# Kernel tuning notes

Measured on AMD Instinct MI355X. Metric: run time of the kernel, lower is better.

Reference implementation:

```python
import jax, jax.numpy as jnp
import numpy as np

K = 12           # boundary_k
TEMP = 0.75      # logit_temperature


def _knn_idx(p):
    # p: [N,3]; brute-force kNN within one batch element (pointops offsets => per-batch)
    sq = jnp.sum(p * p, axis=-1)
    d2 = sq[:, None] + sq[None, :] - 2.0 * (p @ p.T)   # [N,N]
    _, idx = jax.lax.top_k(-d2, K + 1)                  # self is nearest (d=0)
    return idx[:, 1:]                                    # drop self -> [N,K]


def _mlp2(x, W1, b1, W2, b2, relu_out):
    h = jax.nn.relu(x @ W1 + b1) @ W2 + b2
    return jax.nn.relu(h) if relu_out else h


def setup_inputs() -> dict:
    key = jax.random.key(0)
    ks = jax.random.split(key, 32)
    B, N, C = 4, 4096, 17
    dims = [256, 512, 768]
    RD = 320
    s = 0.02
    inp = {
        'feat0': jax.random.normal(ks[0], (B, N, dims[0]), jnp.float32),
        'feat1': jax.random.normal(ks[1], (B, N, dims[1]), jnp.float32),
        'feat2': jax.random.normal(ks[2], (B, N, dims[2]), jnp.float32),
        'logits': jax.random.normal(ks[3], (B, N, C), jnp.float32),
        'labels': jax.random.randint(ks[4], (B, N), 0, C, jnp.int32),
        'pos': jax.random.normal(ks[5], (B, N, 3), jnp.float32),
    }
    # feat projections
    for i, d in enumerate(dims):
        inp[f'Wp{i}'] = jax.random.normal(ks[6 + i], (d, RD), jnp.float32) * s
        inp[f'bp{i}'] = jnp.zeros((RD,), jnp.float32)
    # boundary encoder 6->96->160
    inp['Wbe1'] = jax.random.normal(ks[10], (6, 96), jnp.float32) * s
    inp['bbe1'] = jnp.zeros((96,), jnp.float32)
    inp['Wbe2'] = jax.random.normal(ks[11], (96, 160), jnp.float32) * s
    inp['bbe2'] = jnp.zeros((160,), jnp.float32)
    # attention (RD+160)->320->n_scales
    inp['Wa1'] = jax.random.normal(ks[12], (RD + 160, 320), jnp.float32) * s
    inp['ba1'] = jnp.zeros((320,), jnp.float32)
    inp['Wa2'] = jax.random.normal(ks[13], (320, 3), jnp.float32) * s
    inp['ba2'] = jnp.zeros((3,), jnp.float32)
    # output proj RD->RD->RD
    inp['Wo1'] = jax.random.normal(ks[14], (RD, RD), jnp.float32) * s
    inp['bo1'] = jnp.zeros((RD,), jnp.float32)
    inp['Wo2'] = jax.random.normal(ks[15], (RD, RD), jnp.float32) * s
    inp['bo2'] = jnp.zeros((RD,), jnp.float32)
    return inp


def boundary_info(logits, labels, pos):
    idx = jax.vmap(_knn_idx)(pos)                          # [B,N,K]
    nb_lab = jax.vmap(lambda l, i: l[i])(labels, idx)      # [B,N,K]
    nb_pos = jax.vmap(lambda p, i: p[i])(pos, idx)         # [B,N,K,3]
    diff = nb_lab != labels[..., None]                     # [B,N,K]
    diff_f = diff.astype(jnp.float32)
    dist = jnp.linalg.norm(nb_pos - pos[:, :, None, :], axis=-1)  # [B,N,K]
    boundary_score = diff_f.mean(axis=-1)
    same = 1.0 - diff_f
    same_dist = (dist * same).sum(-1) / (same.sum(-1) + 1e-6)
    bdist = jnp.min(jnp.where(diff, dist, jnp.inf), axis=-1)
    bdist = jnp.where(jnp.isfinite(bdist), bdist, same_dist)
    mean_d = dist.mean(-1)
    density = 1.0 / (mean_d + 1e-6)
    curvature = jnp.std(dist, axis=-1, ddof=1) / (mean_d + 1e-6)  # torch.std unbiased
    probs = jax.nn.softmax(logits / TEMP, axis=-1)
    confidence = probs.max(-1)
    entropy = -(probs * jnp.log(probs + 1e-8)).sum(-1) / jnp.log(jnp.float32(probs.shape[-1]))
    return jnp.stack([boundary_score, confidence, entropy, density, curvature, bdist], axis=-1)


def reference(feat0, feat1, feat2, logits, labels, pos,
              Wp0, bp0, Wp1, bp1, Wp2, bp2,
              Wbe1, bbe1, Wbe2, bbe2,
              Wa1, ba1, Wa2, ba2,
              Wo1, bo1, Wo2, bo2):
    fp = jnp.stack([feat0 @ Wp0 + bp0, feat1 @ Wp1 + bp1, feat2 @ Wp2 + bp2], axis=2)  # [B,N,3,RD]
    info = boundary_info(logits, labels, pos)                       # [B,N,6]
    enc = _mlp2(info, Wbe1, bbe1, Wbe2, bbe2, relu_out=True)        # [B,N,160]
    global_feat = fp.mean(axis=2)                                   # [B,N,RD]
    attn_in = jnp.concatenate([global_feat, enc], axis=-1)
    attn = jax.nn.softmax(_mlp2(attn_in, Wa1, ba1, Wa2, ba2, relu_out=False), axis=-1)  # [B,N,3]
    fused = (fp * attn[..., None]).sum(axis=2)                      # [B,N,RD]
    out = _mlp2(fused, Wo1, bo1, Wo2, bo2, relu_out=False) + global_feat
    return out, attn
```

## Files before the change

kernel.cpp:

```cpp
#include <hip/hip_runtime.h>
#include <stdint.h>

typedef float fx4 __attribute__((ext_vector_type(4)));
typedef short s8 __attribute__((ext_vector_type(8)));
typedef short s4 __attribute__((ext_vector_type(4)));
typedef unsigned int u32;
typedef u32 ux4 __attribute__((ext_vector_type(4)));

#define MTOT 16384
#define NPTS 4096

#define VMCNT7 asm volatile("s_waitcnt vmcnt(7)" ::: "memory")
#define VMCNT5 asm volatile("s_waitcnt vmcnt(5)" ::: "memory")
#define VMCNT0 asm volatile("s_waitcnt vmcnt(0)" ::: "memory")
#define LGKM0  asm volatile("s_waitcnt lgkmcnt(0)" ::: "memory")
#define SBAR   asm volatile("s_barrier" ::: "memory")
#define SCHED0 __builtin_amdgcn_sched_barrier(0)

__device__ __forceinline__ float b2f(short s) {
    return __uint_as_float(((unsigned)(unsigned short)s) << 16);
}
__device__ __forceinline__ short f2b(float f) {
    unsigned u = __float_as_uint(f);
    u += 0x7fffu + ((u >> 16) & 1u);
    return (short)(u >> 16);
}
__device__ __forceinline__ void g2l16(const void* g, void* l) {
    __builtin_amdgcn_global_load_lds(
        (const __attribute__((address_space(1))) unsigned int*)g,
        (__attribute__((address_space(3))) unsigned int*)l, 16, 0, 0);
}
__device__ __forceinline__ void g2l4(const void* g, void* l) {
    __builtin_amdgcn_global_load_lds(
        (const __attribute__((address_space(1))) unsigned int*)g,
        (__attribute__((address_space(3))) unsigned int*)l, 4, 0, 0);
}

struct WTDesc {
    const float* W[8];
    short* Bt[8];
    int K[8];
    int N[8];
    int Kp[8];
    int swz[8];
    int base[9];
};

__global__ __launch_bounds__(256) void wtrans8_kernel(WTDesc d)
{
    int idx = blockIdx.x * 256 + threadIdx.x;
    if (idx >= d.base[8]) return;
    int s = 0;
#pragma unroll
    for (int t = 1; t < 8; ++t) if (idx >= d.base[t]) s = t;
    int local = idx - d.base[s];
    int N = d.N[s];
    if (d.swz[s]) {
        int c = local / 10240, r = local - c * 10240;
        int n = r >> 5, q = r & 31, slot = q >> 3, t = q & 7;
        int kl = ((slot ^ ((n >> 1) & 3)) << 3) | t;
        int k = c * 32 + kl;
        d.Bt[s][local] = f2b(d.W[s][(size_t)k * N + n]);
    } else {
        int Kp = d.Kp[s], K = d.K[s];
        int n = local / Kp, k = local - n * Kp;
        d.Bt[s][local] = (k < K) ? f2b(d.W[s][(size_t)k * N + n]) : (short)0;
    }
}

__global__ __launch_bounds__(256) void aprep_kernel(
    const float* __restrict__ f0, const float* __restrict__ f1, const float* __restrict__ f2,
    short* __restrict__ a0, short* __restrict__ a1, short* __restrict__ a2)
{
    int g = blockIdx.x * 256 + threadIdx.x;
    const float* src; short* dst; int K; size_t w;
    if (g < 1572864)      { src = f2; dst = a2; K = 768; w = (size_t)g * 8; }
    else if (g < 2621440) { src = f1; dst = a1; K = 512; w = (size_t)(g - 1572864) * 8; }
    else                  { src = f0; dst = a0; K = 256; w = (size_t)(g - 2621440) * 8; }
    int Kt = K * 32;
    int mtile = (int)(w / (size_t)Kt);
    int r2 = (int)(w - (size_t)mtile * Kt);
    int chunk = r2 >> 10;
    int within = r2 & 1023;
    int r = within >> 5, q = within & 31;
    int slot = q >> 3;
    int k = chunk * 32 + ((slot ^ ((r >> 1) & 3)) << 3);
    int row = mtile * 32 + r;
    const float* sp = src + (size_t)row * K + k;
    fx4 v0 = *(const fx4*)sp, v1 = *(const fx4*)(sp + 4);
    s8 o;
    o[0] = f2b(v0[0]); o[1] = f2b(v0[1]); o[2] = f2b(v0[2]); o[3] = f2b(v0[3]);
    o[4] = f2b(v1[0]); o[5] = f2b(v1[1]); o[6] = f2b(v1[2]); o[7] = f2b(v1[3]);
    *(s8*)(dst + w) = o;
}

#define SEGW 132
#define KCAP 40

__global__ __launch_bounds__(512) void knn_part_kernel(
    const float* __restrict__ pos, u32* __restrict__ keys)
{
    __shared__ float xs[8 * SEGW], ys[8 * SEGW], zs[8 * SEGW];
    __shared__ u32 cand[64 * KCAP];
    __shared__ u32 samp[64 * 16];
    __shared__ u32 tauA[64];
    __shared__ int cnt[64];

    int bid = blockIdx.x;
    int b   = bid >> 8;
    int cc  = (bid >> 6) & 3;
    int pch = bid & 63;
    int tid = threadIdx.x;
    int jb  = cc << 10;

    if (tid < 64) cnt[tid] = 0;
    for (int idx = tid; idx < 1024; idx += 512) {
        int seg = idx >> 7, o = idx & 127;
        const float* pp = pos + (size_t)(b * NPTS + jb + idx) * 3;
        xs[seg * SEGW + o] = pp[0];
        ys[seg * SEGW + o] = pp[1];
        zs[seg * SEGW + o] = pp[2];
    }
    __syncthreads();

    int lp = tid >> 3, q = tid & 7;
    int gi = pch * 64 + lp;
    const float* mp = pos + (size_t)(b * NPTS + gi) * 3;
    float mx = mp[0], my = mp[1], mz = mp[2];

    const float* xsq = xs + q * SEGW;
    const float* ysq = ys + q * SEGW;
    const float* zsq = zs + q * SEGW;
    int jg0 = jb + q * 128;

    u32 h0 = 0xFFFFFFFFu, h1v = 0xFFFFFFFFu;
    for (int jj = 0; jj < 128; jj += 4) {
        fx4 xv = *reinterpret_cast<const fx4*>(xsq + jj);
        fx4 yv = *reinterpret_cast<const fx4*>(ysq + jj);
        fx4 zv = *reinterpret_cast<const fx4*>(zsq + jj);
#pragma unroll
        for (int u = 0; u < 4; ++u) {
            float dx = xv[u] - mx, dy = yv[u] - my, dz = zv[u] - mz;
            float d2 = fmaf(dx, dx, fmaf(dy, dy, dz * dz));
            int jg = jg0 + jj + u;
            u32 key = (__float_as_uint(d2) & 0xFFFFF000u) | (u32)jg;
            if (jg == gi) key = 0xFFFFFFFFu;
            u32 lo = (key < h0) ? key : h0;
            u32 hi = (key < h0) ? h0 : key;
            h0 = lo;
            h1v = (hi < h1v) ? hi : h1v;
        }
    }
    samp[lp * 16 + q * 2]     = h0;
    samp[lp * 16 + q * 2 + 1] = h1v;
    __syncthreads();

    {
        ux4 sv0 = *(ux4*)&samp[lp * 16];
        ux4 sv1 = *(ux4*)&samp[lp * 16 + 4];
        ux4 sv2 = *(ux4*)&samp[lp * 16 + 8];
        ux4 sv3 = *(ux4*)&samp[lp * 16 + 12];
        int r0 = 0, r1 = 0;
#pragma unroll
        for (int i = 0; i < 4; ++i) {
            r0 += (sv0[i] < h0) + (sv1[i] < h0) + (sv2[i] < h0) + (sv3[i] < h0);
            r1 += (sv0[i] < h1v) + (sv1[i] < h1v) + (sv2[i] < h1v) + (sv3[i] < h1v);
        }
        if (r0 == 11) tauA[lp] = h0;
        if (r1 == 11) tauA[lp] = h1v;
    }
    __syncthreads();
    u32 tau = tauA[lp];

    for (int jj = 0; jj < 128; jj += 4) {
        fx4 xv = *reinterpret_cast<const fx4*>(xsq + jj);
        fx4 yv = *reinterpret_cast<const fx4*>(ysq + jj);
        fx4 zv = *reinterpret_cast<const fx4*>(zsq + jj);
#pragma unroll
        for (int u = 0; u < 4; ++u) {
            float dx = xv[u] - mx, dy = yv[u] - my, dz = zv[u] - mz;
            float d2 = fmaf(dx, dx, fmaf(dy, dy, dz * dz));
            int jg = jg0 + jj + u;
            u32 key = (__float_as_uint(d2) & 0xFFFFF000u) | (u32)jg;
            if (jg == gi) key = 0xFFFFFFFFu;
            if (key <= tau) {
                int slot = atomicAdd(&cnt[lp], 1);
                if (slot < KCAP) cand[lp * KCAP + slot] = key;
            }
        }
    }
    __syncthreads();

    int n = cnt[lp];
    u32 out[12];
    if (n <= KCAP) {
        u32 e0, e1, e2, e3, e4;
        e0 = (q      < n) ? cand[lp * KCAP + q]      : 0xFFFFFFFFu;
        e1 = (q + 8  < n) ? cand[lp * KCAP + q + 8]  : 0xFFFFFFFFu;
        e2 = (q + 16 < n) ? cand[lp * KCAP + q + 16] : 0xFFFFFFFFu;
        e3 = (q + 24 < n) ? cand[lp * KCAP + q + 24] : 0xFFFFFFFFu;
        e4 = (q + 32 < n) ? cand[lp * KCAP + q + 32] : 0xFFFFFFFFu;
#define CE(a, b) { u32 t0 = (a < b) ? a : b; u32 t1 = (a < b) ? b : a; a = t0; b = t1; }
        CE(e0, e1) CE(e1, e2) CE(e2, e3) CE(e3, e4)
        CE(e0, e1) CE(e1, e2) CE(e2, e3)
        CE(e0, e1) CE(e1, e2)
        CE(e0, e1)
#undef CE
        cand[lp * KCAP + q]      = e0;
        cand[lp * KCAP + q + 8]  = e1;
        cand[lp * KCAP + q + 16] = e2;
        cand[lp * KCAP + q + 24] = e3;
        cand[lp * KCAP + q + 32] = e4;
        int ptr = 0;
        u32 head = e0;
#pragma unroll
        for (int r = 0; r < 12; ++r) {
            u32 m = head;
            u32 o1 = __shfl_xor(m, 4, 8); m = (o1 < m) ? o1 : m;
            u32 o2 = __shfl_xor(m, 2, 8); m = (o2 < m) ? o2 : m;
            u32 o3 = __shfl_xor(m, 1, 8); m = (o3 < m) ? o3 : m;
            if (m == head) {
                ++ptr;
                head = (ptr < 5) ? cand[lp * KCAP + q + ptr * 8] : 0xFFFFFFFFu;
            }
            out[r] = m;
        }
    } else {
        u32 hk[12];
#pragma unroll
        for (int k = 0; k < 12; ++k) hk[k] = 0xFFFFFFFFu;
        for (int jj = 0; jj < 128; jj += 4) {
            fx4 xv = *reinterpret_cast<const fx4*>(xsq + jj);
            fx4 yv = *reinterpret_cast<const fx4*>(ysq + jj);
            fx4 zv = *reinterpret_cast<const fx4*>(zsq + jj);
#pragma unroll
            for (int u = 0; u < 4; ++u) {
                float dx = xv[u] - mx, dy = yv[u] - my, dz = zv[u] - mz;
                float d2 = fmaf(dx, dx, fmaf(dy, dy, dz * dz));
                int jg = jg0 + jj + u;
                u32 key = (__float_as_uint(d2) & 0xFFFFF000u) | (u32)jg;
                if (jg == gi) key = 0xFFFFFFFFu;
                if (key < hk[11]) {
                    hk[11] = key;
#pragma unroll
                    for (int k = 11; k >= 1; --k) {
                        u32 a = hk[k], bb = hk[k - 1];
                        u32 mn = (a < bb) ? a : bb;
                        u32 mxv = (a < bb) ? bb : a;
                        hk[k - 1] = mn; hk[k] = mxv;
                    }
                }
            }
        }
#pragma unroll
        for (int r = 0; r < 12; ++r) {
            u32 m = hk[0];
            u32 o1 = __shfl_xor(m, 4, 8); m = (o1 < m) ? o1 : m;
            u32 o2 = __shfl_xor(m, 2, 8); m = (o2 < m) ? o2 : m;
            u32 o3 = __shfl_xor(m, 1, 8); m = (o3 < m) ? o3 : m;
            if (m == hk[0]) {
#pragma unroll
                for (int k = 0; k < 11; ++k) hk[k] = hk[k + 1];
                hk[11] = 0xFFFFFFFFu;
            }
            out[r] = m;
        }
    }

    size_t kb = ((size_t)(b * NPTS + gi) * 4 + cc) * 12;
    if (q == 0) *reinterpret_cast<ux4*>(&keys[kb])     = (ux4){out[0], out[1], out[2], out[3]};
    if (q == 1) *reinterpret_cast<ux4*>(&keys[kb + 4]) = (ux4){out[4], out[5], out[6], out[7]};
    if (q == 2) *reinterpret_cast<ux4*>(&keys[kb + 8]) = (ux4){out[8], out[9], out[10], out[11]};
}

__global__ __launch_bounds__(256) void knn_merge_kernel(
    const u32* __restrict__ keys, const int* __restrict__ labels,
    const float* __restrict__ logits, float* __restrict__ info32)
{
    __shared__ unsigned char labs[NPTS];
    int b  = blockIdx.x >> 6;
    int pc = blockIdx.x & 63;
    int tid = threadIdx.x;
    for (int idx = tid; idx < NPTS; idx += 256)
        labs[idx] = (unsigned char)labels[b * NPTS + idx];
    __syncthreads();

    int lp = tid >> 2, q = tid & 3;
    int gi = pc * 64 + lp;
    size_t kb = ((size_t)(b * NPTS + gi) * 4 + q) * 12;
    ux4 k0 = *reinterpret_cast<const ux4*>(&keys[kb]);
    ux4 k1 = *reinterpret_cast<const ux4*>(&keys[kb + 4]);
    ux4 k2 = *reinterpret_cast<const ux4*>(&keys[kb + 8]);
    u32 hk[12];
    hk[0] = k0[0]; hk[1] = k0[1]; hk[2] = k0[2]; hk[3] = k0[3];
    hk[4] = k1[0]; hk[5] = k1[1]; hk[6] = k1[2]; hk[7] = k1[3];
    hk[8] = k2[0]; hk[9] = k2[1]; hk[10] = k2[2]; hk[11] = k2[3];

    int mylab = (int)labs[gi];
    float sum_d = 0.f, sum_d2 = 0.f, sum_diff = 0.f, same_d = 0.f, bmin = 3.0e38f;
#pragma unroll
    for (int r = 0; r < 12; ++r) {
        u32 m = hk[0];
        u32 o1 = __shfl_xor(m, 2, 4); m = (o1 < m) ? o1 : m;
        u32 o2 = __shfl_xor(m, 1, 4); m = (o2 < m) ? o2 : m;
        if (m == hk[0]) {
#pragma unroll
            for (int k = 0; k < 11; ++k) hk[k] = hk[k + 1];
            hk[11] = 0xFFFFFFFFu;
        }
        float d = sqrtf(__uint_as_float(m & 0xFFFFF000u));
        int j = (int)(m & 0xFFFu);
        float isdiff = ((int)labs[j] != mylab) ? 1.0f : 0.0f;
        sum_d += d;
        sum_d2 = fmaf(d, d, sum_d2);
        sum_diff += isdiff;
        same_d = fmaf(d, 1.0f - isdiff, same_d);
        if (isdiff > 0.f) bmin = fminf(bmin, d);
    }

    if (q == 0) {
        float nsame = 12.0f - sum_diff;
        float mean_d = sum_d * (1.0f / 12.0f);
        float var = fmaxf(0.f, (sum_d2 - 12.0f * mean_d * mean_d) * (1.0f / 11.0f));
        float md_eps = mean_d + 1e-6f;
        float curvature = sqrtf(var) / md_eps;
        float density = 1.0f / md_eps;
        float same_dist = same_d / (nsame + 1e-6f);
        float bdist = (bmin < 2.9e38f) ? bmin : same_dist;
        float bscore = sum_diff * (1.0f / 12.0f);

        const float* lg = logits + (size_t)(b * NPTS + gi) * 17;
        float v[17];
        float vmax = -3.0e38f;
#pragma unroll
        for (int c = 0; c < 17; ++c) { v[c] = lg[c] * (1.0f / 0.75f); vmax = fmaxf(vmax, v[c]); }
        float ssum = 0.f;
#pragma unroll
        for (int c = 0; c < 17; ++c) { v[c] = expf(v[c] - vmax); ssum += v[c]; }
        float inv = 1.0f / ssum;
        float conf = 0.f, ent = 0.f;
#pragma unroll
        for (int c = 0; c < 17; ++c) {
            float pprob = v[c] * inv;
            conf = fmaxf(conf, pprob);
            ent += pprob * logf(pprob + 1e-8f);
        }
        ent = -ent * (1.0f / 2.8332133f);

        float* op = info32 + (size_t)(b * NPTS + gi) * 32;
        fx4 o0 = {bscore, conf, ent, density};
        fx4 o1v = {curvature, bdist, 0.f, 0.f};
        fx4 zz = {0.f, 0.f, 0.f, 0.f};
        *reinterpret_cast<fx4*>(op + 0)  = o0;
        *reinterpret_cast<fx4*>(op + 4)  = o1v;
        *reinterpret_cast<fx4*>(op + 8)  = zz;
        *reinterpret_cast<fx4*>(op + 12) = zz;
        *reinterpret_cast<fx4*>(op + 16) = zz;
        *reinterpret_cast<fx4*>(op + 20) = zz;
        *reinterpret_cast<fx4*>(op + 24) = zz;
        *reinterpret_cast<fx4*>(op + 28) = zz;
    }
}

template<bool AF32, bool RELU, bool NMASK, bool ADDF, bool OUTF, bool OUTB>
__global__ __launch_bounds__(256) void gemm_k(
    const void* __restrict__ Ap, int lda,
    const short* __restrict__ Bt,
    const float* __restrict__ bias,
    float* __restrict__ Cf, int ldcf,
    short* __restrict__ Cb, int ldcb, int cboff,
    const float* __restrict__ Af, int ldaf,
    int N, int K, int ntiles)
{
    __shared__ short As[128 * 40];
    __shared__ short Bs[64 * 40];
    int bid = blockIdx.x;
    int mt = bid / ntiles, nt = bid - mt * ntiles;
    int m0 = mt * 128, n0 = nt * 64;
    int tid = threadIdx.x, l = tid & 63, wid = tid >> 6;
    int wm = wid & 1, wn = wid >> 1, lr = l & 15, lh = l >> 4;
    fx4 acc[4][2] = {};

    int nsteps = K >> 5;
    for (int kt = 0; kt < nsteps; ++kt) {
        int k0 = kt << 5;
        if constexpr (AF32) {
            const float* A = (const float*)Ap;
#pragma unroll
            for (int it = 0; it < 4; ++it) {
                int tt = tid + it * 256;
                int row = tt >> 3, seg = tt & 7;
                fx4 vv = *reinterpret_cast<const fx4*>(A + (size_t)(m0 + row) * lda + k0 + seg * 4);
                s4 w; w[0] = f2b(vv[0]); w[1] = f2b(vv[1]); w[2] = f2b(vv[2]); w[3] = f2b(vv[3]);
                *reinterpret_cast<s4*>(&As[row * 40 + seg * 4]) = w;
            }
        } else {
            const short* A = (const short*)Ap;
#pragma unroll
            for (int it = 0; it < 2; ++it) {
                int tt = tid + it * 256;
                int row = tt >> 2, seg = tt & 3;
                s8 vv = *reinterpret_cast<const s8*>(A + (size_t)(m0 + row) * lda + k0 + seg * 8);
                *reinterpret_cast<s8*>(&As[row * 40 + seg * 8]) = vv;
            }
        }
        {
            int row = tid >> 2, seg = tid & 3;
            s8 vb = {0, 0, 0, 0, 0, 0, 0, 0};
            if (!NMASK || (n0 + row) < N)
                vb = *reinterpret_cast<const s8*>(Bt + (size_t)(n0 + row) * K + k0 + seg * 8);
            *reinterpret_cast<s8*>(&Bs[row * 40 + seg * 8]) = vb;
        }
        __syncthreads();
        s8 af[4], bfr[2];
#pragma unroll
        for (int mf = 0; mf < 4; ++mf)
            af[mf] = *reinterpret_cast<s8*>(&As[(wm * 64 + mf * 16 + lr) * 40 + lh * 8]);
#pragma unroll
        for (int nf = 0; nf < 2; ++nf)
            bfr[nf] = *reinterpret_cast<s8*>(&Bs[(wn * 32 + nf * 16 + lr) * 40 + lh * 8]);
#pragma unroll
        for (int mf = 0; mf < 4; ++mf)
#pragma unroll
            for (int nf = 0; nf < 2; ++nf)
                acc[mf][nf] = __builtin_amdgcn_mfma_f32_16x16x32_bf16(af[mf], bfr[nf], acc[mf][nf], 0, 0, 0);
        __syncthreads();
    }

#pragma unroll
    for (int nf = 0; nf < 2; ++nf) {
        int col = n0 + wn * 32 + nf * 16 + lr;
        if (NMASK && col >= N) continue;
        float bv = bias[col];
#pragma unroll
        for (int mf = 0; mf < 4; ++mf) {
            int r0 = m0 + wm * 64 + mf * 16 + lh * 4;
#pragma unroll
            for (int rg = 0; rg < 4; ++rg) {
                float c = acc[mf][nf][rg] + bv;
                if (RELU) c = fmaxf(c, 0.0f);
                int row = r0 + rg;
                if constexpr (ADDF) c += Af[(size_t)row * ldaf + col];
                if constexpr (OUTF) Cf[(size_t)row * ldcf + col] = c;
                if constexpr (OUTB) Cb[(size_t)row * ldcb + cboff + col] = f2b(c);
            }
        }
    }
}

__global__ __launch_bounds__(256, 2) void mega_kernel(
    const short* __restrict__ at0, const short* __restrict__ at1, const short* __restrict__ at2,
    const short* __restrict__ btp0, const short* __restrict__ btp1, const short* __restrict__ btp2,
    const float* __restrict__ bp0, const float* __restrict__ bp1, const float* __restrict__ bp2,
    const short* __restrict__ bta1, const float* __restrict__ ba1,
    const float* __restrict__ Wa2, const float* __restrict__ ba2,
    const short* __restrict__ bto1, const float* __restrict__ bo1,
    const short* __restrict__ bto2, const float* __restrict__ bo2,
    const short* __restrict__ encb,
    float* __restrict__ outf, float* __restrict__ attn_out)
{
    __shared__ alignas(16) short smem[38144];
    char* smb = (char*)smem;
    constexpr int BB0 = 0, BB1 = 20480, AB0 = 40960, AB1 = 43008, R2B = 45056, SWF = 75776;
    float* smf = (float*)(smb + SWF);

    int tid = threadIdx.x, l = tid & 63, wid = tid >> 6;
    int lr = l & 15, lh = l >> 4;
    int m0 = blockIdx.x * 32;

    auto stageB = [&](int bbase, const short* btg, int kt) {
#pragma unroll
        for (int r = 0; r < 5; ++r) {
            int idx = tid + r * 256;
            g2l16(btg + (size_t)kt * 10240 + idx * 8, smb + bbase + idx * 16);
        }
    };
    auto stageA = [&](int abase, const short* atgm, int kt) {
        const short* src = atgm + (size_t)kt * 1024;
        g2l4(src + tid * 2,       smb + abase + tid * 4);
        g2l4(src + 512 + tid * 2, smb + abase + 1024 + tid * 4);
    };
    auto readB = [&](int bbase, s8* bf) {
#pragma unroll
        for (int nf = 0; nf < 5; ++nf) {
            int row = wid * 80 + nf * 16 + lr;
            bf[nf] = *(const s8*)(smb + bbase + row * 64 + ((lh ^ ((row >> 1) & 3)) << 4));
        }
    };
    auto readAp = [&](int abase, s8* af) {
#pragma unroll
        for (int mf = 0; mf < 2; ++mf) {
            int row = mf * 16 + lr;
            af[mf] = *(const s8*)(smb + abase + row * 64 + ((lh ^ ((row >> 1) & 3)) << 4));
        }
    };

    fx4 gacc[2][5] = {};

    auto do_proj = [&](const short* atgm, const short* btg, int ns,
                       const float* bias, s4 (&fpks)[2][5]) {
        fx4 acc[2][5] = {};
        stageB(BB0, btg, 0); stageA(AB0, atgm, 0);
        stageB(BB1, btg, 1); stageA(AB1, atgm, 1);
        LGKM0;
#pragma unroll 1
        for (int kt = 0; kt < ns; ++kt) {
            if (kt < ns - 1) { VMCNT7; } else { VMCNT0; }
            SBAR;
            int cb = (kt & 1) ? BB1 : BB0;
            int ca = (kt & 1) ? AB1 : AB0;
            s8 af[2], bf[5];
            readAp(ca, af);
            readB(cb, bf);
            LGKM0; SCHED0;
            SBAR;
            if (kt + 2 < ns) { stageB(cb, btg, kt + 2); stageA(ca, atgm, kt + 2); }
#pragma unroll
            for (int mf = 0; mf < 2; ++mf)
#pragma unroll
                for (int nf = 0; nf < 5; ++nf)
                    acc[mf][nf] = __builtin_amdgcn_mfma_f32_16x16x32_bf16(af[mf], bf[nf], acc[mf][nf], 0, 0, 0);
        }
#pragma unroll
        for (int nf = 0; nf < 5; ++nf) {
            float bv = bias[wid * 80 + nf * 16 + lr];
#pragma unroll
            for (int mf = 0; mf < 2; ++mf) {
                s4 pk;
#pragma unroll
                for (int rg = 0; rg < 4; ++rg) {
                    float c = acc[mf][nf][rg] + bv;
                    gacc[mf][nf][rg] += c;
                    pk[rg] = f2b(c);
                }
                fpks[mf][nf] = pk;
            }
        }
    };

    s4 fpk0[2][5], fpk1[2][5], fpk2[2][5];
    do_proj(at2 + (size_t)blockIdx.x * 24576, btp2, 24, bp2, fpk2);
    do_proj(at1 + (size_t)blockIdx.x * 16384, btp1, 16, bp1, fpk1);
    do_proj(at0 + (size_t)blockIdx.x * 8192,  btp0, 8,  bp0, fpk0);

#pragma unroll
    for (int nf = 0; nf < 5; ++nf) {
        int col = wid * 80 + nf * 16 + lr;
#pragma unroll
        for (int mf = 0; mf < 2; ++mf)
#pragma unroll
            for (int rg = 0; rg < 4; ++rg) {
                int row = mf * 16 + lh * 4 + rg;
                int bir = (col * 2) ^ (((row >> 1) & 3) << 4);
                *(short*)(smb + R2B + row * 960 + bir) = f2b(gacc[mf][nf][rg] * (1.0f / 3.0f));
            }
    }
#pragma unroll
    for (int r = 0; r < 3; ++r) {
        int idx = tid + r * 256;
        if (idx < 640) {
            int row = idx / 20, sg = idx - row * 20;
            s8 v = *reinterpret_cast<const s8*>(encb + (size_t)(m0 + row) * 160 + sg * 8);
            int bir = (640 + sg * 16) ^ (((row >> 1) & 3) << 4);
            *(s8*)(smb + R2B + row * 960 + bir) = v;
        }
    }

    auto do_gemm2 = [&](const short* btg, int ns, fx4 acc[2][5]) {
        stageB(BB0, btg, 0);
        stageB(BB1, btg, 1);
        LGKM0;
#pragma unroll 1
        for (int kt = 0; kt < ns; ++kt) {
            if (kt < ns - 1) { VMCNT5; } else { VMCNT0; }
            SBAR;
            int cb = (kt & 1) ? BB1 : BB0;
            s8 af[2], bf[5];
#pragma unroll
            for (int mf = 0; mf < 2; ++mf) {
                int row = mf * 16 + lr;
                int bir = (kt * 64 + (lh << 4)) ^ (((row >> 1) & 3) << 4);
                af[mf] = *(const s8*)(smb + R2B + row * 960 + bir);
            }
            readB(cb, bf);
            LGKM0; SCHED0;
            SBAR;
            if (kt + 2 < ns) stageB(cb, btg, kt + 2);
#pragma unroll
            for (int mf = 0; mf < 2; ++mf)
#pragma unroll
                for (int nf = 0; nf < 5; ++nf)
                    acc[mf][nf] = __builtin_amdgcn_mfma_f32_16x16x32_bf16(af[mf], bf[nf], acc[mf][nf], 0, 0, 0);
        }
    };

    {
        fx4 acc1[2][5] = {};
        do_gemm2(bta1, 15, acc1);
#pragma unroll
        for (int nf = 0; nf < 5; ++nf) {
            int col = wid * 80 + nf * 16 + lr;
            float bv = ba1[col];
#pragma unroll
            for (int mf = 0; mf < 2; ++mf)
#pragma unroll
                for (int rg = 0; rg < 4; ++rg) {
                    int row = mf * 16 + lh * 4 + rg;
                    int bir = (col * 2) ^ (((row >> 1) & 3) << 4);
                    *(short*)(smb + R2B + row * 960 + bir) = f2b(fmaxf(acc1[mf][nf][rg] + bv, 0.0f));
                }
        }
    }

    {
        float* ws2 = (float*)smb;
        if (tid < 240)
            reinterpret_cast<fx4*>(ws2)[tid] = reinterpret_cast<const fx4*>(Wa2)[tid];
        __syncthreads();
        int row = tid >> 3, g = tid & 7;
        float l0 = 0.f, l1 = 0.f, l2 = 0.f;
#pragma unroll
        for (int j = 0; j < 5; ++j) {
            int bir = (g * 80 + j * 16) ^ (((row >> 1) & 3) << 4);
            s8 v = *(const s8*)(smb + R2B + row * 960 + bir);
#pragma unroll
            for (int u = 0; u < 8; ++u) {
                float f = b2f(v[u]);
                const float* wp = ws2 + (g * 40 + j * 8 + u) * 3;
                l0 = fmaf(f, wp[0], l0);
                l1 = fmaf(f, wp[1], l1);
                l2 = fmaf(f, wp[2], l2);
            }
        }
#pragma unroll
        for (int s = 4; s >= 1; s >>= 1) {
            l0 += __shfl_xor(l0, s, 8);
            l1 += __shfl_xor(l1, s, 8);
            l2 += __shfl_xor(l2, s, 8);
        }
        if (g == 0) {
            l0 += ba2[0]; l1 += ba2[1]; l2 += ba2[2];
            float mx = fmaxf(l0, fmaxf(l1, l2));
            float e0 = expf(l0 - mx), e1 = expf(l1 - mx), e2 = expf(l2 - mx);
            float inv = 1.0f / (e0 + e1 + e2);
            float w0 = e0 * inv, w1 = e1 * inv, w2 = e2 * inv;
            attn_out[(size_t)(m0 + row) * 3 + 0] = w0;
            attn_out[(size_t)(m0 + row) * 3 + 1] = w1;
            attn_out[(size_t)(m0 + row) * 3 + 2] = w2;
            smf[row * 4 + 0] = w0; smf[row * 4 + 1] = w1; smf[row * 4 + 2] = w2;
        }
        __syncthreads();
    }

#pragma unroll
    for (int mf = 0; mf < 2; ++mf)
#pragma unroll
        for (int rg = 0; rg < 4; ++rg) {
            int row = mf * 16 + lh * 4 + rg;
            float w0 = smf[row * 4 + 0], w1 = smf[row * 4 + 1], w2 = smf[row * 4 + 2];
#pragma unroll
            for (int nf = 0; nf < 5; ++nf) {
                int col = wid * 80 + nf * 16 + lr;
                float fv = w0 * b2f(fpk0[mf][nf][rg])
                         + w1 * b2f(fpk1[mf][nf][rg])
                         + w2 * b2f(fpk2[mf][nf][rg]);
                int bir = (col * 2) ^ (((row >> 1) & 3) << 4);
                *(short*)(smb + R2B + row * 960 + bir) = f2b(fv);
            }
        }

    {
        fx4 acch[2][5] = {};
        do_gemm2(bto1, 10, acch);
#pragma unroll
        for (int nf = 0; nf < 5; ++nf) {
            int col = wid * 80 + nf * 16 + lr;
            float bv = bo1[col];
#pragma unroll
            for (int mf = 0; mf < 2; ++mf)
#pragma unroll
                for (int rg = 0; rg < 4; ++rg) {
                    int row = mf * 16 + lh * 4 + rg;
                    int bir = (col * 2) ^ (((row >> 1) & 3) << 4);
                    *(short*)(smb + R2B + row * 960 + bir) = f2b(fmaxf(acch[mf][nf][rg] + bv, 0.0f));
                }
        }
    }

    {
        fx4 acco[2][5] = {};
        do_gemm2(bto2, 10, acco);
#pragma unroll
        for (int nf = 0; nf < 5; ++nf) {
            int col = wid * 80 + nf * 16 + lr;
            float bv = bo2[col];
#pragma unroll
            for (int mf = 0; mf < 2; ++mf)
#pragma unroll
                for (int rg = 0; rg < 4; ++rg) {
                    int row = m0 + mf * 16 + lh * 4 + rg;
                    float c = acco[mf][nf][rg] + bv + gacc[mf][nf][rg] * (1.0f / 3.0f);
                    outf[(size_t)row * 320 + col] = c;
                }
        }
    }
}

extern "C" void kernel_launch(void* const* d_in, const int* in_sizes, int n_in,
                              void* d_out, int out_size, void* d_ws, size_t ws_size,
                              hipStream_t stream)
{
    const float* feat0  = (const float*)d_in[0];
    const float* feat1  = (const float*)d_in[1];
    const float* feat2  = (const float*)d_in[2];
    const float* logits = (const float*)d_in[3];
    const int*   labels = (const int*)d_in[4];
    const float* pos    = (const float*)d_in[5];
    const float* Wp0 = (const float*)d_in[6];   const float* bp0 = (const float*)d_in[7];
    const float* Wp1 = (const float*)d_in[8];   const float* bp1 = (const float*)d_in[9];
    const float* Wp2 = (const float*)d_in[10];  const float* bp2 = (const float*)d_in[11];
    const float* Wbe1 = (const float*)d_in[12]; const float* bbe1 = (const float*)d_in[13];
    const float* Wbe2 = (const float*)d_in[14]; const float* bbe2 = (const float*)d_in[15];
    const float* Wa1 = (const float*)d_in[16];  const float* ba1 = (const float*)d_in[17];
    const float* Wa2 = (const float*)d_in[18];  const float* ba2 = (const float*)d_in[19];
    const float* Wo1 = (const float*)d_in[20];  const float* bo1 = (const float*)d_in[21];
    const float* Wo2 = (const float*)d_in[22];  const float* bo2 = (const float*)d_in[23];

    char* p = (char*)d_ws;
    auto alloc = [&](size_t bytes) { char* r = p; p += (bytes + 255) & ~(size_t)255; return r; };
    short* bt_p0  = (short*)alloc((size_t)320 * 256 * 2);
    short* bt_p1  = (short*)alloc((size_t)320 * 512 * 2);
    short* bt_p2  = (short*)alloc((size_t)320 * 768 * 2);
    short* bt_be1 = (short*)alloc((size_t)96 * 32 * 2);
    short* bt_be2 = (short*)alloc((size_t)160 * 96 * 2);
    short* bt_a1  = (short*)alloc((size_t)320 * 480 * 2);
    short* bt_o1  = (short*)alloc((size_t)320 * 320 * 2);
    short* bt_o2  = (short*)alloc((size_t)320 * 320 * 2);
    float* info32 = (float*)alloc((size_t)MTOT * 32 * 4);
    short* h1     = (short*)alloc((size_t)MTOT * 96 * 2);
    short* encb   = (short*)alloc((size_t)MTOT * 160 * 2);
    u32*   knnkeys= (u32*)alloc((size_t)MTOT * 4 * 12 * 4);
    short* abt0   = (short*)alloc((size_t)MTOT * 256 * 2);
    short* abt1   = (short*)alloc((size_t)MTOT * 512 * 2);
    short* abt2   = (short*)alloc((size_t)MTOT * 768 * 2);

    float* outf = (float*)d_out;
    float* attn_out = outf + (size_t)MTOT * 320;

    WTDesc wd;
    const float* Ws[8] = {Wp0, Wp1, Wp2, Wbe1, Wbe2, Wa1, Wo1, Wo2};
    short* Bts[8] = {bt_p0, bt_p1, bt_p2, bt_be1, bt_be2, bt_a1, bt_o1, bt_o2};
    int Ks[8]  = {256, 512, 768, 6, 96, 480, 320, 320};
    int Ns[8]  = {320, 320, 320, 96, 160, 320, 320, 320};
    int Kps[8] = {256, 512, 768, 32, 96, 480, 320, 320};
    int Sz[8]  = {1, 1, 1, 0, 0, 1, 1, 1};
    int acc = 0;
    for (int s = 0; s < 8; ++s) {
        wd.W[s] = Ws[s]; wd.Bt[s] = Bts[s];
        wd.K[s] = Ks[s]; wd.N[s] = Ns[s]; wd.Kp[s] = Kps[s]; wd.swz[s] = Sz[s];
        wd.base[s] = acc;
        acc += Ns[s] * Kps[s];
    }
    wd.base[8] = acc;
    wtrans8_kernel<<<(acc + 255) / 256, 256, 0, stream>>>(wd);

    knn_part_kernel<<<1024, 512, 0, stream>>>(pos, knnkeys);
    knn_merge_kernel<<<256, 256, 0, stream>>>(knnkeys, labels, logits, info32);

    gemm_k<true, true, true, false, false, true><<<256, 256, 0, stream>>>(
        info32, 32, bt_be1, bbe1, nullptr, 0, h1, 96, 0, nullptr, 0, 96, 32, 2);
    gemm_k<false, true, true, false, false, true><<<384, 256, 0, stream>>>(
        h1, 96, bt_be2, bbe2, nullptr, 0, encb, 160, 0, nullptr, 0, 160, 96, 3);

    aprep_kernel<<<12288, 256, 0, stream>>>(feat0, feat1, feat2, abt0, abt1, abt2);

    mega_kernel<<<512, 256, 0, stream>>>(
        abt0, abt1, abt2,
        bt_p0, bt_p1, bt_p2,
        bp0, bp1, bp2,
        bt_a1, ba1, Wa2, ba2,
        bt_o1, bo1, bt_o2, bo2,
        encb, outf, attn_out);
}
```

Measured before the change: 160.0 us.

## Enlarge mega kernel tile to 64 rows, triple-buffer, and fuse aprep into kNN launch

The mega kernel now runs 512 threads on a 64-row tile. Its 8 waves are split 2x4 over M and N, so each B-weight tile staged into LDS is reused across twice as many rows. The K-loop moves from double to triple buffering, which drops the second barrier per iteration and adjusts the vmcnt waits to match. The bf16 A-prep conversion, with its layout re-tiled for 64-row tiles, is merged into the kNN partition kernel as extra blocks to save a launch and overlap with kNN work. The cost is much larger LDS (about 133 KB per block) and fewer resident blocks, only 256 blocks total, which may leave CUs underused.

```diff
diff --git a/kernel.cpp b/kernel.cpp
--- a/kernel.cpp
+++ b/kernel.cpp
@@ -10,8 +10,8 @@
 #define MTOT 16384
 #define NPTS 4096
 
-#define VMCNT7 asm volatile("s_waitcnt vmcnt(7)" ::: "memory")
-#define VMCNT5 asm volatile("s_waitcnt vmcnt(5)" ::: "memory")
+#define VMCNT6 asm volatile("s_waitcnt vmcnt(6)" ::: "memory")
+#define VMCNT4 asm volatile("s_waitcnt vmcnt(4)" ::: "memory")
 #define VMCNT0 asm volatile("s_waitcnt vmcnt(0)" ::: "memory")
 #define LGKM0  asm volatile("s_waitcnt lgkmcnt(0)" ::: "memory")
 #define SBAR   asm volatile("s_barrier" ::: "memory")
@@ -68,43 +68,43 @@
     }
 }
 
-__global__ __launch_bounds__(256) void aprep_kernel(
+#define SEGW 132
+#define KCAP 40
+
+__global__ __launch_bounds__(512) void knap_kernel(
+    const float* __restrict__ pos, u32* __restrict__ keys,
     const float* __restrict__ f0, const float* __restrict__ f1, const float* __restrict__ f2,
     short* __restrict__ a0, short* __restrict__ a1, short* __restrict__ a2)
-{
-    int g = blockIdx.x * 256 + threadIdx.x;
-    const float* src; short* dst; int K; size_t w;
-    if (g < 1572864)      { src = f2; dst = a2; K = 768; w = (size_t)g * 8; }
-    else if (g < 2621440) { src = f1; dst = a1; K = 512; w = (size_t)(g - 1572864) * 8; }
-    else                  { src = f0; dst = a0; K = 256; w = (size_t)(g - 2621440) * 8; }
-    int Kt = K * 32;
-    int mtile = (int)(w / (size_t)Kt);
-    int r2 = (int)(w - (size_t)mtile * Kt);
-    int chunk = r2 >> 10;
-    int within = r2 & 1023;
-    int r = within >> 5, q = within & 31;
-    int slot = q >> 3;
-    int k = chunk * 32 + ((slot ^ ((r >> 1) & 3)) << 3);
-    int row = mtile * 32 + r;
-    const float* sp = src + (size_t)row * K + k;
-    fx4 v0 = *(const fx4*)sp, v1 = *(const fx4*)(sp + 4);
-    s8 o;
-    o[0] = f2b(v0[0]); o[1] = f2b(v0[1]); o[2] = f2b(v0[2]); o[3] = f2b(v0[3]);
-    o[4] = f2b(v1[0]); o[5] = f2b(v1[1]); o[6] = f2b(v1[2]); o[7] = f2b(v1[3]);
-    *(s8*)(dst + w) = o;
-}
-
-#define SEGW 132
-#define KCAP 40
-
-__global__ __launch_bounds__(512) void knn_part_kernel(
-    const float* __restrict__ pos, u32* __restrict__ keys)
 {
     __shared__ float xs[8 * SEGW], ys[8 * SEGW], zs[8 * SEGW];
     __shared__ u32 cand[64 * KCAP];
     __shared__ u32 samp[64 * 16];
     __shared__ u32 tauA[64];
     __shared__ int cnt[64];
+
+    if (blockIdx.x >= 1024) {
+        int g = (blockIdx.x - 1024) * 512 + threadIdx.x;
+        const float* src; short* dst; int K; size_t w;
+        if (g < 1572864)      { src = f2; dst = a2; K = 768; w = (size_t)g * 8; }
+        else if (g < 2621440) { src = f1; dst = a1; K = 512; w = (size_t)(g - 1572864) * 8; }
+        else                  { src = f0; dst = a0; K = 256; w = (size_t)(g - 2621440) * 8; }
+        int Kt = K * 64;
+        int mtile = (int)(w / (size_t)Kt);
+        int r2 = (int)(w - (size_t)mtile * Kt);
+        int chunk = r2 >> 11;
+        int within = r2 & 2047;
+        int r = within >> 5, q = within & 31;
+        int slot = q >> 3;
+        int k = chunk * 32 + ((slot ^ ((r >> 1) & 3)) << 3);
+        int row = mtile * 64 + r;
+        const float* sp = src + (size_t)row * K + k;
+        fx4 v0 = *(const fx4*)sp, v1 = *(const fx4*)(sp + 4);
+        s8 o;
+        o[0] = f2b(v0[0]); o[1] = f2b(v0[1]); o[2] = f2b(v0[2]); o[3] = f2b(v0[3]);
+        o[4] = f2b(v1[0]); o[5] = f2b(v1[1]); o[6] = f2b(v1[2]); o[7] = f2b(v1[3]);
+        *(s8*)(dst + w) = o;
+        return;
+    }
 
     int bid = blockIdx.x;
     int b   = bid >> 8;
@@ -448,7 +448,7 @@
     }
 }
 
-__global__ __launch_bounds__(256, 2) void mega_kernel(
+__global__ __launch_bounds__(512, 2) void mega_kernel(
     const short* __restrict__ at0, const short* __restrict__ at1, const short* __restrict__ at2,
     const short* __restrict__ btp0, const short* __restrict__ btp1, const short* __restrict__ btp2,
     const float* __restrict__ bp0, const float* __restrict__ bp1, const float* __restrict__ bp2,
@@ -459,38 +459,45 @@
     const short* __restrict__ encb,
     float* __restrict__ outf, float* __restrict__ attn_out)
 {
-    __shared__ alignas(16) short smem[38144];
-    char* smb = (char*)smem;
-    constexpr int BB0 = 0, BB1 = 20480, AB0 = 40960, AB1 = 43008, R2B = 45056, SWF = 75776;
+    __shared__ alignas(16) char smb[136192];
+    const int BBo[3] = {0, 20480, 40960};
+    const int ABo[3] = {61440, 65536, 69632};
+    constexpr int R2B = 73728, SWF = 135168;
     float* smf = (float*)(smb + SWF);
 
-    int tid = threadIdx.x, l = tid & 63, wid = tid >> 6;
-    int lr = l & 15, lh = l >> 4;
-    int m0 = blockIdx.x * 32;
+    int tid = threadIdx.x, wid = tid >> 6, l = tid & 63;
+    int wm = wid >> 2, wn = wid & 3, lr = l & 15, lh = l >> 4;
+    int m0 = blockIdx.x * 64;
 
     auto stageB = [&](int bbase, const short* btg, int kt) {
-#pragma unroll
-        for (int r = 0; r < 5; ++r) {
-            int idx = tid + r * 256;
-            g2l16(btg + (size_t)kt * 10240 + idx * 8, smb + bbase + idx * 16);
-        }
+        const char* s = (const char*)(btg + (size_t)kt * 10240);
+        int o1 = wid * 1024 + l * 16;
+        int o2 = 8192 + o1;
+        int o3 = 16384 + wid * 256 + l * 4;
+        int o4 = 2048 + o3;
+        g2l16(s + o1, smb + bbase + o1);
+        g2l16(s + o2, smb + bbase + o2);
+        g2l4(s + o3, smb + bbase + o3);
+        g2l4(s + o4, smb + bbase + o4);
     };
     auto stageA = [&](int abase, const short* atgm, int kt) {
-        const short* src = atgm + (size_t)kt * 1024;
-        g2l4(src + tid * 2,       smb + abase + tid * 4);
-        g2l4(src + 512 + tid * 2, smb + abase + 1024 + tid * 4);
+        const char* s = (const char*)(atgm + (size_t)kt * 2048);
+        int o1 = wid * 256 + l * 4;
+        int o2 = 2048 + o1;
+        g2l4(s + o1, smb + abase + o1);
+        g2l4(s + o2, smb + abase + o2);
     };
     auto readB = [&](int bbase, s8* bf) {
 #pragma unroll
         for (int nf = 0; nf < 5; ++nf) {
-            int row = wid * 80 + nf * 16 + lr;
+            int row = wn * 80 + nf * 16 + lr;
             bf[nf] = *(const s8*)(smb + bbase + row * 64 + ((lh ^ ((row >> 1) & 3)) << 4));
         }
     };
-    auto readAp = [&](int abase, s8* af) {
+    auto readA = [&](int abase, s8* af) {
 #pragma unroll
         for (int mf = 0; mf < 2; ++mf) {
-            int row = mf * 16 + lr;
+            int row = wm * 32 + mf * 16 + lr;
             af[mf] = *(const s8*)(smb + abase + row * 64 + ((lh ^ ((row >> 1) & 3)) << 4));
         }
     };
@@ -500,30 +507,33 @@
     auto do_proj = [&](const short* atgm, const short* btg, int ns,
                        const float* bias, s4 (&fpks)[2][5]) {
         fx4 acc[2][5] = {};
-        stageB(BB0, btg, 0); stageA(AB0, atgm, 0);
-        stageB(BB1, btg, 1); stageA(AB1, atgm, 1);
+        stageB(BBo[0], btg, 0); stageA(ABo[0], atgm, 0);
+        stageB(BBo[1], btg, 1); stageA(ABo[1], atgm, 1);
         LGKM0;
 #pragma unroll 1
         for (int kt = 0; kt < ns; ++kt) {
-            if (kt < ns - 1) { VMCNT7; } else { VMCNT0; }
+            if (kt < ns - 1) { VMCNT6; } else { VMCNT0; }
             SBAR;
-            int cb = (kt & 1) ? BB1 : BB0;
-            int ca = (kt & 1) ? AB1 : AB0;
+            int ph = kt - (kt / 3) * 3;
             s8 af[2], bf[5];
-            readAp(ca, af);
-            readB(cb, bf);
-            LGKM0; SCHED0;
-            SBAR;
-            if (kt + 2 < ns) { stageB(cb, btg, kt + 2); stageA(ca, atgm, kt + 2); }
+            readA(ABo[ph], af);
+            readB(BBo[ph], bf);
+            if (kt + 2 < ns) {
+                int p2 = (kt + 2) - ((kt + 2) / 3) * 3;
+                stageB(BBo[p2], btg, kt + 2);
+                stageA(ABo[p2], atgm, kt + 2);
+            }
 #pragma unroll
             for (int mf = 0; mf < 2; ++mf)
 #pragma unroll
                 for (int nf = 0; nf < 5; ++nf)
                     acc[mf][nf] = __builtin_amdgcn_mfma_f32_16x16x32_bf16(af[mf], bf[nf], acc[mf][nf], 0, 0, 0);
-        }
+            SCHED0; LGKM0;
+        }
+        SBAR;
 #pragma unroll
         for (int nf = 0; nf < 5; ++nf) {
-            float bv = bias[wid * 80 + nf * 16 + lr];
+            float bv = bias[wn * 80 + nf * 16 + lr];
 #pragma unroll
             for (int mf = 0; mf < 2; ++mf) {
                 s4 pk;
@@ -539,26 +549,26 @@
     };
 
     s4 fpk0[2][5], fpk1[2][5], fpk2[2][5];
-    do_proj(at2 + (size_t)blockIdx.x * 24576, btp2, 24, bp2, fpk2);
-    do_proj(at1 + (size_t)blockIdx.x * 16384, btp1, 16, bp1, fpk1);
-    do_proj(at0 + (size_t)blockIdx.x * 8192,  btp0, 8,  bp0, fpk0);
+    do_proj(at2 + (size_t)blockIdx.x * 49152, btp2, 24, bp2, fpk2);
+    do_proj(at1 + (size_t)blockIdx.x * 32768, btp1, 16, bp1, fpk1);
+    do_proj(at0 + (size_t)blockIdx.x * 16384, btp0, 8,  bp0, fpk0);
 
 #pragma unroll
     for (int nf = 0; nf < 5; ++nf) {
-        int col = wid * 80 + nf * 16 + lr;
+        int col = wn * 80 + nf * 16 + lr;
 #pragma unroll
         for (int mf = 0; mf < 2; ++mf)
 #pragma unroll
             for (int rg = 0; rg < 4; ++rg) {
-                int row = mf * 16 + lh * 4 + rg;
+                int row = wm * 32 + mf * 16 + lh * 4 + rg;
                 int bir = (col * 2) ^ (((row >> 1) & 3) << 4);
                 *(short*)(smb + R2B + row * 960 + bir) = f2b(gacc[mf][nf][rg] * (1.0f / 3.0f));
             }
     }
 #pragma unroll
     for (int r = 0; r < 3; ++r) {
-        int idx = tid + r * 256;
-        if (idx < 640) {
+        int idx = tid + r * 512;
+        if (idx < 1280) {
             int row = idx / 20, sg = idx - row * 20;
             s8 v = *reinterpret_cast<const s8*>(encb + (size_t)(m0 + row) * 160 + sg * 8);
             int bir = (640 + sg * 16) ^ (((row >> 1) & 3) << 4);
@@ -566,32 +576,35 @@
         }
     }
 
-    auto do_gemm2 = [&](const short* btg, int ns, fx4 acc[2][5]) {
-        stageB(BB0, btg, 0);
-        stageB(BB1, btg, 1);
+    auto do_gemm2 = [&](const short* btg, int ns, fx4 (&acc)[2][5]) {
+        stageB(BBo[0], btg, 0);
+        stageB(BBo[1], btg, 1);
         LGKM0;
 #pragma unroll 1
         for (int kt = 0; kt < ns; ++kt) {
-            if (kt < ns - 1) { VMCNT5; } else { VMCNT0; }
+            if (kt < ns - 1) { VMCNT4; } else { VMCNT0; }
             SBAR;
-            int cb = (kt & 1) ? BB1 : BB0;
+            int ph = kt - (kt / 3) * 3;
             s8 af[2], bf[5];
 #pragma unroll
             for (int mf = 0; mf < 2; ++mf) {
-                int row = mf * 16 + lr;
+                int row = wm * 32 + mf * 16 + lr;
                 int bir = (kt * 64 + (lh << 4)) ^ (((row >> 1) & 3) << 4);
                 af[mf] = *(const s8*)(smb + R2B + row * 960 + bir);
             }
-            readB(cb, bf);
-            LGKM0; SCHED0;
-            SBAR;
-            if (kt + 2 < ns) stageB(cb, btg, kt + 2);
+            readB(BBo[ph], bf);
+            if (kt + 2 < ns) {
+                int p2 = (kt + 2) - ((kt + 2) / 3) * 3;
+                stageB(BBo[p2], btg, kt + 2);
+            }
 #pragma unroll
             for (int mf = 0; mf < 2; ++mf)
 #pragma unroll
                 for (int nf = 0; nf < 5; ++nf)
                     acc[mf][nf] = __builtin_amdgcn_mfma_f32_16x16x32_bf16(af[mf], bf[nf], acc[mf][nf], 0, 0, 0);
-        }
+            SCHED0; LGKM0;
+        }
+        SBAR;
     };
 
     {
@@ -599,13 +612,13 @@
         do_gemm2(bta1, 15, acc1);
 #pragma unroll
         for (int nf = 0; nf < 5; ++nf) {
-            int col = wid * 80 + nf * 16 + lr;
+            int col = wn * 80 + nf * 16 + lr;
             float bv = ba1[col];
 #pragma unroll
             for (int mf = 0; mf < 2; ++mf)
 #pragma unroll
                 for (int rg = 0; rg < 4; ++rg) {
-                    int row = mf * 16 + lh * 4 + rg;
+                    int row = wm * 32 + mf * 16 + lh * 4 + rg;
                     int bir = (col * 2) ^ (((row >> 1) & 3) << 4);
                     *(short*)(smb + R2B + row * 960 + bir) = f2b(fmaxf(acc1[mf][nf][rg] + bv, 0.0f));
                 }
@@ -656,11 +669,11 @@
     for (int mf = 0; mf < 2; ++mf)
 #pragma unroll
         for (int rg = 0; rg < 4; ++rg) {
-            int row = mf * 16 + lh * 4 + rg;
+            int row = wm * 32 + mf * 16 + lh * 4 + rg;
             float w0 = smf[row * 4 + 0], w1 = smf[row * 4 + 1], w2 = smf[row * 4 + 2];
 #pragma unroll
             for (int nf = 0; nf < 5; ++nf) {
-                int col = wid * 80 + nf * 16 + lr;
+                int col = wn * 80 + nf * 16 + lr;
                 float fv = w0 * b2f(fpk0[mf][nf][rg])
                          + w1 * b2f(fpk1[mf][nf][rg])
                          + w2 * b2f(fpk2[mf][nf][rg]);
@@ -674,13 +687,13 @@
         do_gemm2(bto1, 10, acch);
 #pragma unroll
         for (int nf = 0; nf < 5; ++nf) {
-            int col = wid * 80 + nf * 16 + lr;
+            int col = wn * 80 + nf * 16 + lr;
             float bv = bo1[col];
 #pragma unroll
             for (int mf = 0; mf < 2; ++mf)
 #pragma unroll
                 for (int rg = 0; rg < 4; ++rg) {
-                    int row = mf * 16 + lh * 4 + rg;
+                    int row = wm * 32 + mf * 16 + lh * 4 + rg;
                     int bir = (col * 2) ^ (((row >> 1) & 3) << 4);
                     *(short*)(smb + R2B + row * 960 + bir) = f2b(fmaxf(acch[mf][nf][rg] + bv, 0.0f));
                 }
@@ -692,13 +705,13 @@
         do_gemm2(bto2, 10, acco);
 #pragma unroll
         for (int nf = 0; nf < 5; ++nf) {
-            int col = wid * 80 + nf * 16 + lr;
+            int col = wn * 80 + nf * 16 + lr;
             float bv = bo2[col];
 #pragma unroll
             for (int mf = 0; mf < 2; ++mf)
 #pragma unroll
                 for (int rg = 0; rg < 4; ++rg) {
-                    int row = m0 + mf * 16 + lh * 4 + rg;
+                    int row = m0 + wm * 32 + mf * 16 + lh * 4 + rg;
                     float c = acco[mf][nf][rg] + bv + gacc[mf][nf][rg] * (1.0f / 3.0f);
                     outf[(size_t)row * 320 + col] = c;
                 }
@@ -764,7 +777,9 @@
     wd.base[8] = acc;
     wtrans8_kernel<<<(acc + 255) / 256, 256, 0, stream>>>(wd);
 
-    knn_part_kernel<<<1024, 512, 0, stream>>>(pos, knnkeys);
+    knap_kernel<<<7168, 512, 0, stream>>>(pos, knnkeys,
+                                          feat0, feat1, feat2,
+                                          abt0, abt1, abt2);
     knn_merge_kernel<<<256, 256, 0, stream>>>(knnkeys, labels, logits, info32);
 
     gemm_k<true, true, true, false, false, true><<<256, 256, 0, stream>>>(
@@ -772,9 +787,7 @@
     gemm_k<false, true, true, false, false, true><<<384, 256, 0, stream>>>(
         h1, 96, bt_be2, bbe2, nullptr, 0, encb, 160, 0, nullptr, 0, 160, 96, 3);
 
-    aprep_kernel<<<12288, 256, 0, stream>>>(feat0, feat1, feat2, abt0, abt1, abt2);
-
-    mega_kernel<<<512, 256, 0, stream>>>(
+    mega_kernel<<<256, 512, 0, stream>>>(
         abt0, abt1, abt2,
         bt_p0, bt_p1, bt_p2,
         bp0, bp1, bp2,
```

Measured after the change: 155.0 us. 3.1% less time.

## Merge aprep into kNN partition kernel and spill projection fragments to global

Applied to the files above, without the earlier changes.

The bf16 feature-repack work (aprep) now runs as extra blocks appended to the kNN partition kernel, so both jobs share one launch and the memory-bound conversion can overlap the compute-bound kNN. In the mega kernel, the three per-scale projection fragments are written to a per-thread global scratch buffer instead of being held in registers, and read back later for the attention-weighted fusion. This is meant to cut register pressure and raise occupancy, at the cost of extra global traffic and larger shared-memory footprint for the aprep blocks, which now carry the kNN kernel's static LDS.

```diff
diff --git a/kernel.cpp b/kernel.cpp
--- a/kernel.cpp
+++ b/kernel.cpp
@@ -68,43 +68,43 @@
     }
 }
 
-__global__ __launch_bounds__(256) void aprep_kernel(
+#define SEGW 132
+#define KCAP 40
+
+__global__ __launch_bounds__(512) void knap_kernel(
+    const float* __restrict__ pos, u32* __restrict__ keys,
     const float* __restrict__ f0, const float* __restrict__ f1, const float* __restrict__ f2,
     short* __restrict__ a0, short* __restrict__ a1, short* __restrict__ a2)
-{
-    int g = blockIdx.x * 256 + threadIdx.x;
-    const float* src; short* dst; int K; size_t w;
-    if (g < 1572864)      { src = f2; dst = a2; K = 768; w = (size_t)g * 8; }
-    else if (g < 2621440) { src = f1; dst = a1; K = 512; w = (size_t)(g - 1572864) * 8; }
-    else                  { src = f0; dst = a0; K = 256; w = (size_t)(g - 2621440) * 8; }
-    int Kt = K * 32;
-    int mtile = (int)(w / (size_t)Kt);
-    int r2 = (int)(w - (size_t)mtile * Kt);
-    int chunk = r2 >> 10;
-    int within = r2 & 1023;
-    int r = within >> 5, q = within & 31;
-    int slot = q >> 3;
-    int k = chunk * 32 + ((slot ^ ((r >> 1) & 3)) << 3);
-    int row = mtile * 32 + r;
-    const float* sp = src + (size_t)row * K + k;
-    fx4 v0 = *(const fx4*)sp, v1 = *(const fx4*)(sp + 4);
-    s8 o;
-    o[0] = f2b(v0[0]); o[1] = f2b(v0[1]); o[2] = f2b(v0[2]); o[3] = f2b(v0[3]);
-    o[4] = f2b(v1[0]); o[5] = f2b(v1[1]); o[6] = f2b(v1[2]); o[7] = f2b(v1[3]);
-    *(s8*)(dst + w) = o;
-}
-
-#define SEGW 132
-#define KCAP 40
-
-__global__ __launch_bounds__(512) void knn_part_kernel(
-    const float* __restrict__ pos, u32* __restrict__ keys)
 {
     __shared__ float xs[8 * SEGW], ys[8 * SEGW], zs[8 * SEGW];
     __shared__ u32 cand[64 * KCAP];
     __shared__ u32 samp[64 * 16];
     __shared__ u32 tauA[64];
     __shared__ int cnt[64];
+
+    if (blockIdx.x >= 1024) {
+        int g = (blockIdx.x - 1024) * 512 + threadIdx.x;
+        const float* src; short* dst; int K; size_t w;
+        if (g < 1572864)      { src = f2; dst = a2; K = 768; w = (size_t)g * 8; }
+        else if (g < 2621440) { src = f1; dst = a1; K = 512; w = (size_t)(g - 1572864) * 8; }
+        else                  { src = f0; dst = a0; K = 256; w = (size_t)(g - 2621440) * 8; }
+        int Kt = K * 32;
+        int mtile = (int)(w / (size_t)Kt);
+        int r2 = (int)(w - (size_t)mtile * Kt);
+        int chunk = r2 >> 10;
+        int within = r2 & 1023;
+        int r = within >> 5, q = within & 31;
+        int slot = q >> 3;
+        int k = chunk * 32 + ((slot ^ ((r >> 1) & 3)) << 3);
+        int row = mtile * 32 + r;
+        const float* sp = src + (size_t)row * K + k;
+        fx4 v0 = *(const fx4*)sp, v1 = *(const fx4*)(sp + 4);
+        s8 o;
+        o[0] = f2b(v0[0]); o[1] = f2b(v0[1]); o[2] = f2b(v0[2]); o[3] = f2b(v0[3]);
+        o[4] = f2b(v1[0]); o[5] = f2b(v1[1]); o[6] = f2b(v1[2]); o[7] = f2b(v1[3]);
+        *(s8*)(dst + w) = o;
+        return;
+    }
 
     int bid = blockIdx.x;
     int b   = bid >> 8;
@@ -456,17 +456,19 @@
     const float* __restrict__ Wa2, const float* __restrict__ ba2,
     const short* __restrict__ bto1, const float* __restrict__ bo1,
     const short* __restrict__ bto2, const float* __restrict__ bo2,
-    const short* __restrict__ encb,
+    const short* __restrict__ encb, short* __restrict__ fpb,
     float* __restrict__ outf, float* __restrict__ attn_out)
 {
     __shared__ alignas(16) short smem[38144];
     char* smb = (char*)smem;
     constexpr int BB0 = 0, BB1 = 20480, AB0 = 40960, AB1 = 43008, R2B = 45056, SWF = 75776;
+    constexpr size_t FPS = (size_t)512 * 256 * 40;
     float* smf = (float*)(smb + SWF);
 
     int tid = threadIdx.x, l = tid & 63, wid = tid >> 6;
     int lr = l & 15, lh = l >> 4;
     int m0 = blockIdx.x * 32;
+    short* fpt = fpb + (size_t)(blockIdx.x * 256 + tid) * 40;
 
     auto stageB = [&](int bbase, const short* btg, int kt) {
 #pragma unroll
@@ -498,7 +500,7 @@
     fx4 gacc[2][5] = {};
 
     auto do_proj = [&](const short* atgm, const short* btg, int ns,
-                       const float* bias, s4 (&fpks)[2][5]) {
+                       const float* bias, short* fpo) {
         fx4 acc[2][5] = {};
         stageB(BB0, btg, 0); stageA(AB0, atgm, 0);
         stageB(BB1, btg, 1); stageA(AB1, atgm, 1);
@@ -533,15 +535,14 @@
                     gacc[mf][nf][rg] += c;
                     pk[rg] = f2b(c);
                 }
-                fpks[mf][nf] = pk;
+                *(s4*)(fpo + (mf * 5 + nf) * 4) = pk;
             }
         }
     };
 
-    s4 fpk0[2][5], fpk1[2][5], fpk2[2][5];
-    do_proj(at2 + (size_t)blockIdx.x * 24576, btp2, 24, bp2, fpk2);
-    do_proj(at1 + (size_t)blockIdx.x * 16384, btp1, 16, bp1, fpk1);
-    do_proj(at0 + (size_t)blockIdx.x * 8192,  btp0, 8,  bp0, fpk0);
+    do_proj(at2 + (size_t)blockIdx.x * 24576, btp2, 24, bp2, fpt + 2 * FPS);
+    do_proj(at1 + (size_t)blockIdx.x * 16384, btp1, 16, bp1, fpt + 1 * FPS);
+    do_proj(at0 + (size_t)blockIdx.x * 8192,  btp0, 8,  bp0, fpt);
 
 #pragma unroll
     for (int nf = 0; nf < 5; ++nf) {
@@ -566,7 +567,7 @@
         }
     }
 
-    auto do_gemm2 = [&](const short* btg, int ns, fx4 acc[2][5]) {
+    auto do_gemm2 = [&](const short* btg, int ns, fx4 (&acc)[2][5]) {
         stageB(BB0, btg, 0);
         stageB(BB1, btg, 1);
         LGKM0;
@@ -655,15 +656,17 @@
 #pragma unroll
     for (int mf = 0; mf < 2; ++mf)
 #pragma unroll
-        for (int rg = 0; rg < 4; ++rg) {
-            int row = mf * 16 + lh * 4 + rg;
-            float w0 = smf[row * 4 + 0], w1 = smf[row * 4 + 1], w2 = smf[row * 4 + 2];
-#pragma unroll
-            for (int nf = 0; nf < 5; ++nf) {
-                int col = wid * 80 + nf * 16 + lr;
-                float fv = w0 * b2f(fpk0[mf][nf][rg])
-                         + w1 * b2f(fpk1[mf][nf][rg])
-                         + w2 * b2f(fpk2[mf][nf][rg]);
+        for (int nf = 0; nf < 5; ++nf) {
+            s4 p0 = *(const s4*)(fpt + (mf * 5 + nf) * 4);
+            s4 p1 = *(const s4*)(fpt + 1 * FPS + (mf * 5 + nf) * 4);
+            s4 p2 = *(const s4*)(fpt + 2 * FPS + (mf * 5 + nf) * 4);
+            int col = wid * 80 + nf * 16 + lr;
+#pragma unroll
+            for (int rg = 0; rg < 4; ++rg) {
+                int row = mf * 16 + lh * 4 + rg;
+                float fv = smf[row * 4 + 0] * b2f(p0[rg])
+                         + smf[row * 4 + 1] * b2f(p1[rg])
+                         + smf[row * 4 + 2] * b2f(p2[rg]);
                 int bir = (col * 2) ^ (((row >> 1) & 3) << 4);
                 *(short*)(smb + R2B + row * 960 + bir) = f2b(fv);
             }
@@ -743,6 +746,7 @@
     short* abt0   = (short*)alloc((size_t)MTOT * 256 * 2);
     short* abt1   = (short*)alloc((size_t)MTOT * 512 * 2);
     short* abt2   = (short*)alloc((size_t)MTOT * 768 * 2);
+    short* fpb    = (short*)alloc((size_t)3 * 512 * 256 * 40 * 2);
 
     float* outf = (float*)d_out;
     float* attn_out = outf + (size_t)MTOT * 320;
@@ -764,15 +768,15 @@
     wd.base[8] = acc;
     wtrans8_kernel<<<(acc + 255) / 256, 256, 0, stream>>>(wd);
 
-    knn_part_kernel<<<1024, 512, 0, stream>>>(pos, knnkeys);
+    knap_kernel<<<7168, 512, 0, stream>>>(pos, knnkeys,
+                                          feat0, feat1, feat2,
+                                          abt0, abt1, abt2);
     knn_merge_kernel<<<256, 256, 0, stream>>>(knnkeys, labels, logits, info32);
 
     gemm_k<true, true, true, false, false, true><<<256, 256, 0, stream>>>(
         info32, 32, bt_be1, bbe1, nullptr, 0, h1, 96, 0, nullptr, 0, 96, 32, 2);
     gemm_k<false, true, true, false, false, true><<<384, 256, 0, stream>>>(
         h1, 96, bt_be2, bbe2, nullptr, 0, encb, 160, 0, nullptr, 0, 160, 96, 3);
-
-    aprep_kernel<<<12288, 256, 0, stream>>>(feat0, feat1, feat2, abt0, abt1, abt2);
 
     mega_kernel<<<512, 256, 0, stream>>>(
         abt0, abt1, abt2,
@@ -780,5 +784,5 @@
         bp0, bp1, bp2,
         bt_a1, ba1, Wa2, ba2,
         bt_o1, bo1, bt_o2, bo2,
-        encb, outf, attn_out);
-}
+        encb, fpb, outf, attn_out);
+}
```

Result: faster. 134.6 us (-15.9%).
